# Performance work log

Measured on AMD Instinct MI355X. Metric: run time of the kernel, lower is better.

Reference implementation:

```python
import jax, jax.numpy as jnp
import numpy as np

EPS = 0.01
BETA = 0.8
GAMMA_A = 0.01
GAMMA_W = 0.01
ALPHA = 1.0
N_UNITS = 128

def setup_inputs() -> dict:
    key = jax.random.key(0)
    ks = jax.random.split(key, 7)
    B, T, D_in, C_out = 512, 1024, 64, 10
    return {
        "x": jax.random.normal(ks[0], (B, T, D_in), dtype=jnp.float32),
        "E_w": jax.random.normal(ks[1], (N_UNITS, D_in), dtype=jnp.float32) / np.sqrt(D_in),
        "E_b": jax.random.normal(ks[2], (N_UNITS,), dtype=jnp.float32) * 0.01,
        "B_p": jax.random.normal(ks[3], (N_UNITS, N_UNITS), dtype=jnp.float32) / N_UNITS,
        "C_p": jax.random.normal(ks[4], (N_UNITS, N_UNITS), dtype=jnp.float32) / N_UNITS,
        "D_w": jax.random.normal(ks[5], (C_out, N_UNITS), dtype=jnp.float32) / np.sqrt(N_UNITS),
        "D_b": jax.random.normal(ks[6], (C_out,), dtype=jnp.float32) * 0.01,
    }

def reference(x, E_w, E_b, B_p, C_p, D_w, D_b):
    B, T, _ = x.shape
    I = jnp.eye(N_UNITS, dtype=x.dtype)
    # Skew/symmetric mixture recurrent matrices (computed once, as in i==0 branch)
    A = BETA * (B_p - B_p.T) + (1.0 - BETA) * (B_p + B_p.T) - GAMMA_A * I
    W = BETA * (C_p - C_p.T) + (1.0 - BETA) * (C_p + C_p.T) - GAMMA_W * I
    # Input projection for all timesteps at once: [T, B, n_units]
    Z = jnp.einsum('bti,ui->tbu', x, E_w) + E_b
    h0 = jnp.zeros((B, N_UNITS), dtype=x.dtype)

    def step(h, z):
        h_update = ALPHA * (h @ A) + jnp.tanh(h @ W + z)
        return h + EPS * h_update, None

    h_final, _ = jax.lax.scan(step, h0, Z)
    return h_final @ D_w.T + D_b
```

## Files before the change

### kernel.cpp

```cpp
#include <hip/hip_runtime.h>

#define EPS_C 0.01f
#define NU    128
#define DIN   64
#define COUT  10

typedef float    f32x4 __attribute__((ext_vector_type(4)));
typedef _Float16 f16x4 __attribute__((ext_vector_type(4)));
typedef _Float16 f16x8 __attribute__((ext_vector_type(8)));

#define MFMA32(A, B, C) __builtin_amdgcn_mfma_f32_16x16x32_f16((A), (B), (C), 0, 0, 0)
#define BAR() asm volatile("s_waitcnt lgkmcnt(0)\n\ts_barrier" ::: "memory")

__global__ __launch_bounds__(512, 1)
void rnn_core(const float* __restrict__ x,
              const float* __restrict__ E_w, const float* __restrict__ E_b,
              const float* __restrict__ B_p, const float* __restrict__ C_p,
              const float* __restrict__ D_w, const float* __restrict__ D_b,
              float* __restrict__ out, int T)
{
    const int tid  = threadIdx.x;
    const int lane = tid & 63;
    const int w    = tid >> 6;
    const int lid  = lane & 15;
    const int q    = lane >> 4;
    const int g    = blockIdx.x;

    __shared__ _Float16 xs[2][16 * 2 * 64 * 8];
    __shared__ _Float16 hbuf[2][4][64][8];
    __shared__ float    hfin[16][NU + 4];

    f16x8 AT[4], WT[4], EF[2];
    f32x4 ebv;
    {
        const int m = w * 16 + lid;
        #pragma unroll
        for (int kt = 0; kt < 4; ++kt) {
            f16x8 fa, fw;
            #pragma unroll
            for (int j = 0; j < 8; ++j) {
                const int k  = kt * 32 + q * 8 + j;
                const float dg = (k == m) ? 0.01f : 0.0f;
                fa[j] = (_Float16)(B_p[k * NU + m] - 0.6f * B_p[m * NU + k] - dg);
                fw[j] = (_Float16)(C_p[k * NU + m] - 0.6f * C_p[m * NU + k] - dg);
            }
            AT[kt] = fa;  WT[kt] = fw;
        }
        #pragma unroll
        for (int kt = 0; kt < 2; ++kt) {
            f16x8 fe;
            #pragma unroll
            for (int j = 0; j < 8; ++j)
                fe[j] = (_Float16)E_w[m * DIN + kt * 32 + q * 8 + j];
            EF[kt] = fe;
        }
        #pragma unroll
        for (int r = 0; r < 4; ++r)
            ebv[r] = E_b[w * 16 + q * 4 + r];
    }

    const int bb = tid & 15;
    const int s2 = (tid >> 4) & 15;
    const int tp = tid >> 8;
    const float* xrow = x + ((size_t)(g * 16 + bb) * T) * DIN + s2 * 4;
    const int wb2 = (((s2 >> 3) * 64) + (((s2 >> 1) & 3) * 16) + bb) * 16 + (s2 & 1) * 8;

    float4 xg[8];

#define STAGE_WRITE(BUF)                                                      \
    {                                                                         \
        char* base_ = (char*)&xs[(BUF)][0];                                   \
        _Pragma("unroll")                                                     \
        for (int i2 = 0; i2 < 8; ++i2) {                                      \
            float4 v_ = xg[i2];                                               \
            f16x4 h4_;                                                        \
            h4_[0] = (_Float16)v_.x; h4_[1] = (_Float16)v_.y;                 \
            h4_[2] = (_Float16)v_.z; h4_[3] = (_Float16)v_.w;                 \
            *(f16x4*)(base_ + (2 * i2 + tp) * 2048 + wb2) = h4_;              \
        }                                                                     \
    }

    if (tid < 256)
        ((float4*)&hbuf[0][0][0][0])[tid] = (float4){0.f, 0.f, 0.f, 0.f};
    #pragma unroll
    for (int i = 0; i < 8; ++i)
        xg[i] = *(const float4*)(xrow + (size_t)(2 * i + tp) * DIN);
    STAGE_WRITE(0)
    __syncthreads();

    f32x4 hf = {0.f, 0.f, 0.f, 0.f};
    f32x4 zc;
    {
        f16x8 x0 = *(const f16x8*)((char*)&xs[0][0] + (0 * 64 + lane) * 16);
        f16x8 x1 = *(const f16x8*)((char*)&xs[0][0] + (1 * 64 + lane) * 16);
        zc = ebv;
        zc = MFMA32(EF[0], x0, zc);
        zc = MFMA32(EF[1], x1, zc);
    }

    const int nch = T >> 4;
    for (int c = 0; c < nch; ++c) {
        if (c + 1 < nch) {
            const float* xr2 = xrow + (size_t)(c + 1) * 16 * DIN;
            #pragma unroll
            for (int i = 0; i < 8; ++i)
                xg[i] = *(const float4*)(xr2 + (size_t)(2 * i + tp) * DIN);
        }
        #pragma unroll
        for (int i = 0; i < 16; ++i) {
            const int t  = c * 16 + i;
            const int p  = i & 1;
            const int np = p ^ 1;

            f16x8 hB[4];
            #pragma unroll
            for (int kt = 0; kt < 4; ++kt)
                hB[kt] = *(const f16x8*)((char*)&hbuf[p][0][0][0] + (kt * 64 + lane) * 16);

            int tt = t + 1; if (tt >= T) tt = T - 1;
            const int it = tt & 15;
            char* xb = (char*)&xs[(tt >> 4) & 1][0];
            f16x8 xfA = *(const f16x8*)(xb + ((it * 2 + 0) * 64 + lane) * 16);
            f16x8 xfB = *(const f16x8*)(xb + ((it * 2 + 1) * 64 + lane) * 16);

            f32x4 ya = {0.f, 0.f, 0.f, 0.f};
            f32x4 wa = zc;
            #pragma unroll
            for (int kt = 0; kt < 4; ++kt) {
                ya = MFMA32(AT[kt], hB[kt], ya);
                wa = MFMA32(WT[kt], hB[kt], wa);
            }

            {
                f16x4 nh;
                #pragma unroll
                for (int r = 0; r < 4; ++r) {
                    const float arg = wa[r];
                    const float e2  = __expf(2.0f * arg);
                    const float th  = 1.0f - 2.0f * __builtin_amdgcn_rcpf(e2 + 1.0f);
                    const float hv  = hf[r] + EPS_C * (ya[r] + th);
                    hf[r] = hv;
                    nh[r] = (_Float16)hv;
                }
                char* hwp = (char*)&hbuf[np][w >> 1][0][0];
                const int row = (2 * (w & 1) + (q >> 1)) * 16 + lid;
                *(f16x4*)(hwp + row * 16 + (q & 1) * 8) = nh;
            }

            f32x4 zn = ebv;
            zn = MFMA32(EF[0], xfA, zn);
            zn = MFMA32(EF[1], xfB, zn);
            zc = zn;

            if (i == 13 && c + 1 < nch) STAGE_WRITE((c + 1) & 1)
            BAR();
        }
    }

    #pragma unroll
    for (int r = 0; r < 4; ++r)
        hfin[lid][w * 16 + q * 4 + r] = hf[r];
    __syncthreads();

    if (tid < 16 * COUT) {
        const int r  = tid / COUT;
        const int cc = tid - r * COUT;
        float acc = D_b[cc];
        #pragma unroll 8
        for (int u = 0; u < NU; ++u)
            acc = fmaf(hfin[r][u], D_w[cc * NU + u], acc);
        out[((size_t)g * 16 + r) * COUT + cc] = acc;
    }
}

extern "C" void kernel_launch(void* const* d_in, const int* in_sizes, int n_in,
                              void* d_out, int out_size, void* d_ws, size_t ws_size,
                              hipStream_t stream)
{
    const float* x   = (const float*)d_in[0];
    const float* E_w = (const float*)d_in[1];
    const float* E_b = (const float*)d_in[2];
    const float* B_p = (const float*)d_in[3];
    const float* C_p = (const float*)d_in[4];
    const float* D_w = (const float*)d_in[5];
    const float* D_b = (const float*)d_in[6];
    float* out = (float*)d_out;

    const int B  = out_size / COUT;
    const int T  = in_sizes[0] / (B * DIN);
    const int NB = B / 16;

    rnn_core<<<NB, 512, 0, stream>>>(x, E_w, E_b, B_p, C_p, D_w, D_b, out, T);
}
```

Before: 597.7 us.

## Halve block to 4 waves, each computing two 16-unit output tiles

```diff
diff --git a/kernel.cpp b/kernel.cpp
--- a/kernel.cpp
+++ b/kernel.cpp
@@ -12,7 +12,7 @@
 #define MFMA32(A, B, C) __builtin_amdgcn_mfma_f32_16x16x32_f16((A), (B), (C), 0, 0, 0)
 #define BAR() asm volatile("s_waitcnt lgkmcnt(0)\n\ts_barrier" ::: "memory")
 
-__global__ __launch_bounds__(512, 1)
+__global__ __launch_bounds__(256, 1)
 void rnn_core(const float* __restrict__ x,
               const float* __restrict__ E_w, const float* __restrict__ E_b,
               const float* __restrict__ B_p, const float* __restrict__ C_p,
@@ -26,14 +26,15 @@
     const int q    = lane >> 4;
     const int g    = blockIdx.x;
 
-    __shared__ _Float16 xs[2][16 * 2 * 64 * 8];
-    __shared__ _Float16 hbuf[2][4][64][8];
-    __shared__ float    hfin[16][NU + 4];
-
-    f16x8 AT[4], WT[4], EF[2];
-    f32x4 ebv;
-    {
-        const int m = w * 16 + lid;
+    __shared__ __attribute__((aligned(16))) _Float16 xs[2][8 * 1024];
+    __shared__ __attribute__((aligned(16))) _Float16 hbuf[2][4][64][8];
+    __shared__ float hfin[16][NU + 4];
+
+    f16x8 AT[2][4], WT[2][4], EF[2][2];
+    f32x4 ebv[2];
+    #pragma unroll
+    for (int mt = 0; mt < 2; ++mt) {
+        const int m = w * 32 + mt * 16 + lid;
         #pragma unroll
         for (int kt = 0; kt < 4; ++kt) {
             f16x8 fa, fw;
@@ -44,7 +45,7 @@
                 fa[j] = (_Float16)(B_p[k * NU + m] - 0.6f * B_p[m * NU + k] - dg);
                 fw[j] = (_Float16)(C_p[k * NU + m] - 0.6f * C_p[m * NU + k] - dg);
             }
-            AT[kt] = fa;  WT[kt] = fw;
+            AT[mt][kt] = fa;  WT[mt][kt] = fw;
         }
         #pragma unroll
         for (int kt = 0; kt < 2; ++kt) {
@@ -52,16 +53,15 @@
             #pragma unroll
             for (int j = 0; j < 8; ++j)
                 fe[j] = (_Float16)E_w[m * DIN + kt * 32 + q * 8 + j];
-            EF[kt] = fe;
+            EF[mt][kt] = fe;
         }
         #pragma unroll
         for (int r = 0; r < 4; ++r)
-            ebv[r] = E_b[w * 16 + q * 4 + r];
+            ebv[mt][r] = E_b[w * 32 + mt * 16 + q * 4 + r];
     }
 
     const int bb = tid & 15;
-    const int s2 = (tid >> 4) & 15;
-    const int tp = tid >> 8;
+    const int s2 = tid >> 4;
     const float* xrow = x + ((size_t)(g * 16 + bb) * T) * DIN + s2 * 4;
     const int wb2 = (((s2 >> 3) * 64) + (((s2 >> 1) & 3) * 16) + bb) * 16 + (s2 & 1) * 8;
 
@@ -76,90 +76,104 @@
             f16x4 h4_;                                                        \
             h4_[0] = (_Float16)v_.x; h4_[1] = (_Float16)v_.y;                 \
             h4_[2] = (_Float16)v_.z; h4_[3] = (_Float16)v_.w;                 \
-            *(f16x4*)(base_ + (2 * i2 + tp) * 2048 + wb2) = h4_;              \
+            *(f16x4*)(base_ + i2 * 2048 + wb2) = h4_;                         \
         }                                                                     \
     }
 
-    if (tid < 256)
-        ((float4*)&hbuf[0][0][0][0])[tid] = (float4){0.f, 0.f, 0.f, 0.f};
+    ((float4*)&hbuf[0][0][0][0])[tid] = (float4){0.f, 0.f, 0.f, 0.f};
     #pragma unroll
     for (int i = 0; i < 8; ++i)
-        xg[i] = *(const float4*)(xrow + (size_t)(2 * i + tp) * DIN);
+        xg[i] = *(const float4*)(xrow + (size_t)i * DIN);
     STAGE_WRITE(0)
     __syncthreads();
 
-    f32x4 hf = {0.f, 0.f, 0.f, 0.f};
-    f32x4 zc;
+    char* xsb = (char*)&xs[0][0] + lane * 16;
+    char* hrb = (char*)&hbuf[0][0][0][0] + lane * 16;
+    char* hwb = (char*)&hbuf[0][0][0][0]
+              + (w * 64 + (q >> 1) * 16 + lid) * 16 + (q & 1) * 8;
+
+    f32x4 hf[2] = {{0.f,0.f,0.f,0.f}, {0.f,0.f,0.f,0.f}};
+    f32x4 zc0, zc1;
     {
-        f16x8 x0 = *(const f16x8*)((char*)&xs[0][0] + (0 * 64 + lane) * 16);
-        f16x8 x1 = *(const f16x8*)((char*)&xs[0][0] + (1 * 64 + lane) * 16);
-        zc = ebv;
-        zc = MFMA32(EF[0], x0, zc);
-        zc = MFMA32(EF[1], x1, zc);
-    }
-
-    const int nch = T >> 4;
+        f16x8 x0 = *(const f16x8*)(xsb);
+        f16x8 x1 = *(const f16x8*)(xsb + 1024);
+        zc0 = ebv[0];
+        zc0 = MFMA32(EF[0][0], x0, zc0);
+        zc0 = MFMA32(EF[0][1], x1, zc0);
+        zc1 = ebv[1];
+        zc1 = MFMA32(EF[1][0], x0, zc1);
+        zc1 = MFMA32(EF[1][1], x1, zc1);
+    }
+
+    const int nch = T >> 3;
     for (int c = 0; c < nch; ++c) {
         if (c + 1 < nch) {
-            const float* xr2 = xrow + (size_t)(c + 1) * 16 * DIN;
+            const float* xr2 = xrow + (size_t)(c + 1) * 8 * DIN;
             #pragma unroll
             for (int i = 0; i < 8; ++i)
-                xg[i] = *(const float4*)(xr2 + (size_t)(2 * i + tp) * DIN);
-        }
-        #pragma unroll
-        for (int i = 0; i < 16; ++i) {
-            const int t  = c * 16 + i;
+                xg[i] = *(const float4*)(xr2 + (size_t)i * DIN);
+        }
+        #pragma unroll
+        for (int i = 0; i < 8; ++i) {
+            const int t  = c * 8 + i;
             const int p  = i & 1;
             const int np = p ^ 1;
 
             f16x8 hB[4];
             #pragma unroll
             for (int kt = 0; kt < 4; ++kt)
-                hB[kt] = *(const f16x8*)((char*)&hbuf[p][0][0][0] + (kt * 64 + lane) * 16);
+                hB[kt] = *(const f16x8*)(hrb + p * 4096 + kt * 1024);
 
             int tt = t + 1; if (tt >= T) tt = T - 1;
-            const int it = tt & 15;
-            char* xb = (char*)&xs[(tt >> 4) & 1][0];
-            f16x8 xfA = *(const f16x8*)(xb + ((it * 2 + 0) * 64 + lane) * 16);
-            f16x8 xfB = *(const f16x8*)(xb + ((it * 2 + 1) * 64 + lane) * 16);
-
-            f32x4 ya = {0.f, 0.f, 0.f, 0.f};
-            f32x4 wa = zc;
+            char* xb = xsb + ((tt >> 3) & 1) * 16384 + (tt & 7) * 2048;
+            f16x8 xfA = *(const f16x8*)(xb);
+            f16x8 xfB = *(const f16x8*)(xb + 1024);
+
+            f32x4 wa0 = zc0, wa1 = zc1;
             #pragma unroll
             for (int kt = 0; kt < 4; ++kt) {
-                ya = MFMA32(AT[kt], hB[kt], ya);
-                wa = MFMA32(WT[kt], hB[kt], wa);
-            }
-
-            {
+                wa0 = MFMA32(WT[0][kt], hB[kt], wa0);
+                wa1 = MFMA32(WT[1][kt], hB[kt], wa1);
+            }
+            f32x4 ya0 = {0.f,0.f,0.f,0.f}, ya1 = {0.f,0.f,0.f,0.f};
+            #pragma unroll
+            for (int kt = 0; kt < 4; ++kt) {
+                ya0 = MFMA32(AT[0][kt], hB[kt], ya0);
+                ya1 = MFMA32(AT[1][kt], hB[kt], ya1);
+            }
+            f32x4 zn0 = ebv[0], zn1 = ebv[1];
+            zn0 = MFMA32(EF[0][0], xfA, zn0);
+            zn1 = MFMA32(EF[1][0], xfA, zn1);
+            zn0 = MFMA32(EF[0][1], xfB, zn0);
+            zn1 = MFMA32(EF[1][1], xfB, zn1);
+
+            #pragma unroll
+            for (int mt = 0; mt < 2; ++mt) {
+                f32x4 wa = mt ? wa1 : wa0;
+                f32x4 ya = mt ? ya1 : ya0;
                 f16x4 nh;
                 #pragma unroll
                 for (int r = 0; r < 4; ++r) {
-                    const float arg = wa[r];
-                    const float e2  = __expf(2.0f * arg);
-                    const float th  = 1.0f - 2.0f * __builtin_amdgcn_rcpf(e2 + 1.0f);
-                    const float hv  = hf[r] + EPS_C * (ya[r] + th);
-                    hf[r] = hv;
+                    const float e2 = __builtin_amdgcn_exp2f(wa[r] * 2.8853900817779268f);
+                    const float th = 1.0f - 2.0f * __builtin_amdgcn_rcpf(e2 + 1.0f);
+                    const float hv = hf[mt][r] + EPS_C * (ya[r] + th);
+                    hf[mt][r] = hv;
                     nh[r] = (_Float16)hv;
                 }
-                char* hwp = (char*)&hbuf[np][w >> 1][0][0];
-                const int row = (2 * (w & 1) + (q >> 1)) * 16 + lid;
-                *(f16x4*)(hwp + row * 16 + (q & 1) * 8) = nh;
-            }
-
-            f32x4 zn = ebv;
-            zn = MFMA32(EF[0], xfA, zn);
-            zn = MFMA32(EF[1], xfB, zn);
-            zc = zn;
-
-            if (i == 13 && c + 1 < nch) STAGE_WRITE((c + 1) & 1)
+                *(f16x4*)(hwb + np * 4096 + mt * 512) = nh;
+            }
+            zc0 = zn0; zc1 = zn1;
+
+            if (i == 5 && c + 1 < nch) STAGE_WRITE((c + 1) & 1)
             BAR();
         }
     }
 
     #pragma unroll
-    for (int r = 0; r < 4; ++r)
-        hfin[lid][w * 16 + q * 4 + r] = hf[r];
+    for (int mt = 0; mt < 2; ++mt)
+        #pragma unroll
+        for (int r = 0; r < 4; ++r)
+            hfin[lid][w * 32 + mt * 16 + q * 4 + r] = hf[mt][r];
     __syncthreads();
 
     if (tid < 16 * COUT) {
@@ -190,5 +204,5 @@
     const int T  = in_sizes[0] / (B * DIN);
     const int NB = B / 16;
 
-    rnn_core<<<NB, 512, 0, stream>>>(x, E_w, E_b, B_p, C_p, D_w, D_b, out, T);
+    rnn_core<<<NB, 256, 0, stream>>>(x, E_w, E_b, B_p, C_p, D_w, D_b, out, T);
 }
```

After: 588.1 us. No clear change (-1.6%).
